# Optimization experiments

Hardware: AMD Instinct MI355X
Metric: run time of the kernel (lower is better)

Reference implementation:

```python
import jax, jax.numpy as jnp
import numpy as np

# e2m1 FP4 value table: sign bit in nibble MSB, values {0,0.5,1,1.5,2,3,4,6}
_E2M1 = jnp.array([0.0, 0.5, 1.0, 1.5, 2.0, 3.0, 4.0, 6.0,
                   -0.0, -0.5, -1.0, -1.5, -2.0, -3.0, -4.0, -6.0], dtype=jnp.float32)


def _dequant_fp4(packed, scales, group_size):
    """packed: [E, out, in//8] uint32; scales: [E, in//group_size, out] -> [E, out, in] f32."""
    shifts = jnp.arange(8, dtype=jnp.uint32) * 4  # nibble shift amounts 0,4,...,28
    nib = (packed[..., None] >> shifts) & jnp.uint32(0xF)  # [E, out, in//8, 8]
    E, O, P, _ = nib.shape
    nib = nib.reshape(E, O, P * 8).astype(jnp.int32)
    w = _E2M1[nib]  # [E, out, in] f32
    gids = jnp.arange(P * 8) // group_size  # group id per input column
    sc = jnp.transpose(scales, (0, 2, 1))[:, :, gids]  # [E, out, in]
    return w * sc


def setup_inputs() -> dict:
    E, H, I, T, K, G = 8, 2048, 1408, 2048, 2, 128
    key = jax.random.key(0)
    ks = jax.random.split(key, 9)
    x = jax.random.normal(ks[0], (T, H), dtype=jnp.float32)
    gate_packed = jax.random.bits(ks[1], (E, I, H // 8), dtype=jnp.uint32)
    up_packed = jax.random.bits(ks[2], (E, I, H // 8), dtype=jnp.uint32)
    down_packed = jax.random.bits(ks[3], (E, H, I // 8), dtype=jnp.uint32)
    gate_scales = jax.random.uniform(ks[4], (E, H // G, I), jnp.float32, 0.5, 1.5)
    up_scales = jax.random.uniform(ks[5], (E, H // G, I), jnp.float32, 0.5, 1.5)
    down_scales = jax.random.uniform(ks[6], (E, I // G, H), jnp.float32, 0.5, 1.5)
    topk_idx = jax.random.randint(ks[7], (T, K), 0, E, dtype=jnp.int32)
    w = jax.random.uniform(ks[8], (T, K), jnp.float32)
    topk_w = w / jnp.sum(w, axis=-1, keepdims=True)
    return {"x": x,
            "gate_packed": gate_packed, "gate_scales": gate_scales,
            "up_packed": up_packed, "up_scales": up_scales,
            "down_packed": down_packed, "down_scales": down_scales,
            "topk_idx": topk_idx, "topk_w": topk_w, "group_size": G}


def reference(x, gate_packed, gate_scales, up_packed, up_scales,
              down_packed, down_scales, topk_idx, topk_w, group_size):
    # Fused dequant (nibble unpack + e2m1 table + per-group scale) for all experts
    gate_w = _dequant_fp4(gate_packed, gate_scales, group_size)  # [E, I, H]
    up_w = _dequant_fp4(up_packed, up_scales, group_size)        # [E, I, H]
    down_w = _dequant_fp4(down_packed, down_scales, group_size)  # [E, H, I]
    # Grouped SwiGLU expert MLP (dense over E=8 experts, gather routed outputs)
    g = jnp.einsum('th,eih->eti', x, gate_w)
    u = jnp.einsum('th,eih->eti', x, up_w)
    h = jax.nn.silu(g) * u                                        # [E, T, I]
    y = jnp.einsum('eti,ehi->eth', h, down_w)                     # [E, T, H]
    T = x.shape[0]
    sel = y[topk_idx, jnp.arange(T)[:, None], :]                  # [T, K, H]
    return jnp.sum(sel * topk_w[..., None], axis=1)               # [T, H]
```

## Files before the change

kernel.cpp:

```cpp
#include <hip/hip_runtime.h>
#include <hip/hip_bf16.h>
#include <stdint.h>

#define E_ 8
#define H_ 2048
#define I_ 1408
#define T_ 2048
#define K_ 2
#define G_ 128

typedef __bf16 bf16;
typedef bf16 bf16x8 __attribute__((ext_vector_type(8)));
typedef float f32x4 __attribute__((ext_vector_type(4)));

__device__ __forceinline__ uint32_t prm(uint32_t hi, uint32_t lo, uint32_t sel) {
    return __builtin_amdgcn_perm(hi, lo, sel);
}

struct DequantTab { uint32_t thi0, thi1, tlo0, tlo1; };

__device__ __forceinline__ DequantTab build_tab(float s) {
    union { bf16 h[8]; uint32_t u[4]; } tb;
    tb.h[0] = (bf16)(0.0f);
    tb.h[1] = (bf16)(0.5f * s);
    tb.h[2] = (bf16)(1.0f * s);
    tb.h[3] = (bf16)(1.5f * s);
    tb.h[4] = (bf16)(2.0f * s);
    tb.h[5] = (bf16)(3.0f * s);
    tb.h[6] = (bf16)(4.0f * s);
    tb.h[7] = (bf16)(6.0f * s);
    DequantTab t;
    t.thi0 = prm(tb.u[1], tb.u[0], 0x07050301u);
    t.tlo0 = prm(tb.u[1], tb.u[0], 0x06040200u);
    t.thi1 = prm(tb.u[3], tb.u[2], 0x07050301u);
    t.tlo1 = prm(tb.u[3], tb.u[2], 0x06040200u);
    return t;
}

__device__ __forceinline__ uint4 dequant8t(uint32_t p, const DequantTab& t) {
    const uint32_t pr = p >> 4;
    const uint32_t pe = p  & 0x07070707u;
    const uint32_t po = pr & 0x07070707u;
    const uint32_t He = prm(t.thi1, t.thi0, pe) | ((p  & 0x08080808u) << 4);
    const uint32_t Le = prm(t.tlo1, t.tlo0, pe);
    const uint32_t Ho = prm(t.thi1, t.thi0, po) | ((pr & 0x08080808u) << 4);
    const uint32_t Lo = prm(t.tlo1, t.tlo0, po);
    const uint32_t E01 = prm(He, Le, 0x05010400u);
    const uint32_t E23 = prm(He, Le, 0x07030602u);
    const uint32_t O01 = prm(Ho, Lo, 0x05010400u);
    const uint32_t O23 = prm(Ho, Lo, 0x07030602u);
    return make_uint4(prm(O01, E01, 0x05040100u),
                      prm(O01, E01, 0x07060302u),
                      prm(O23, E23, 0x05040100u),
                      prm(O23, E23, 0x07060302u));
}

__device__ __forceinline__ void gld16(void* lds, const void* g) {
    __builtin_amdgcn_global_load_lds(
        (__attribute__((address_space(1))) void*)g,
        (__attribute__((address_space(3))) void*)lds, 16, 0, 0);
}

__global__ void route_count(const int* __restrict__ topk_idx, int* __restrict__ counts) {
    int p = blockIdx.x * blockDim.x + threadIdx.x;
    if (p < T_ * K_) atomicAdd(&counts[topk_idx[p]], 1);
}

__global__ void route_scan(const int* __restrict__ counts, int* __restrict__ offsets,
                           int* __restrict__ tmap) {
    if (threadIdx.x == 0) {
        int acc = 0, ti = 0;
        for (int e = 0; e < E_; e++) {
            offsets[e] = acc;
            int nt = (counts[e] + 127) >> 7;
            for (int j = 0; j < nt; j++) tmap[ti++] = (e << 16) | j;
            acc += counts[e];
        }
        offsets[E_] = acc;
        for (; ti < 64; ti++) tmap[ti] = -1;
    }
}

__global__ void route_fill(const int* __restrict__ topk_idx, const float* __restrict__ topk_w,
                           int* __restrict__ cursors, const int* __restrict__ offsets,
                           int* __restrict__ tok, float* __restrict__ wgt,
                           int* __restrict__ inv) {
    int p = blockIdx.x * blockDim.x + threadIdx.x;
    if (p < T_ * K_) {
        int e = topk_idx[p];
        int slot = atomicAdd(&cursors[e], 1);
        int idx = offsets[e] + slot;
        tok[idx] = p / K_;
        wgt[idx] = topk_w[p];
        inv[p] = idx;
    }
}

__global__ __launch_bounds__(256)
void xcast_kernel(const float* __restrict__ x, uint4* __restrict__ xb) {
    const int i = blockIdx.x * 256 + threadIdx.x;
    const float4 a = ((const float4*)x)[i * 2];
    const float4 b = ((const float4*)x)[i * 2 + 1];
    union { uint4 u; bf16 h[8]; } r;
    r.h[0] = (bf16)a.x; r.h[1] = (bf16)a.y; r.h[2] = (bf16)a.z; r.h[3] = (bf16)a.w;
    r.h[4] = (bf16)b.x; r.h[5] = (bf16)b.y; r.h[6] = (bf16)b.z; r.h[7] = (bf16)b.w;
    xb[i] = r.u;
}

__global__ __launch_bounds__(256, 3)
void gemm1t_kernel(const bf16* __restrict__ xb,
                   const uint32_t* __restrict__ gate_packed,
                   const float* __restrict__ gate_scales,
                   const uint32_t* __restrict__ up_packed,
                   const float* __restrict__ up_scales,
                   const int* __restrict__ offsets,
                   const int* __restrict__ tmap,
                   const int* __restrict__ tok, bf16* __restrict__ h_buf)
{
    const int tm = tmap[blockIdx.x];
    if (tm < 0) return;
    const int e = tm >> 16, ty = tm & 0xffff;
    const int row0 = offsets[e];
    const int cnt = offsets[e + 1] - row0;
    const int itile = blockIdx.y;

    __shared__ __align__(16) bf16 xs[2][128][64];
    __shared__ __align__(16) bf16 wgs[64][64];
    __shared__ __align__(16) bf16 wus[64][64];

    const int tid = threadIdx.x;

    const int xr = tid >> 3;
    const int xc = tid & 7;
    const int xch = (xc ^ (xr & 7)) * 8;
    const bf16* xsrc[4];
    bf16* xdst[4];
#pragma unroll
    for (int j = 0; j < 4; ++j) {
        int g = ty * 128 + xr + j * 32;
        g = (g < cnt) ? g : (cnt - 1);
        xsrc[j] = xb + (size_t)tok[row0 + g] * H_ + xch;
        xdst[j] = &xs[0][xr + j * 32][xc * 8];
    }

    const int mat  = tid >> 7;
    const int id   = tid & 127;
    const int wrow = id >> 1;
    const int quad = id & 1;
    const int irow = itile * 64 + wrow;
    const uint32_t* wp_row = (mat ? up_packed : gate_packed)
        + (size_t)e * I_ * (H_ / 8) + (size_t)irow * (H_ / 8) + quad * 4;
    const float* ws_row = (mat ? up_scales : gate_scales)
        + (size_t)e * (H_ / G_) * I_ + irow;
    bf16 (* const wdst)[64] = mat ? wus : wgs;

    const int wave = tid >> 6, lane = tid & 63;
    const int wy = wave >> 1, wx = wave & 1;
    const int lrow = lane & 15, kq = lane >> 4;

    f32x4 accg[4][2] = {};
    f32x4 accu[4][2] = {};

    float sc_cur = ws_row[0];
    uint4 pw = *(const uint4*)(wp_row);
#pragma unroll
    for (int j = 0; j < 4; ++j) gld16(xdst[j], xsrc[j]);

    constexpr int NG = H_ / G_;
    constexpr int NT = 2 * NG;
    for (int kg = 0; kg < NG; ++kg) {
        const int kgn = (kg + 1 < NG) ? kg + 1 : kg;
        const float sc_nxt = ws_row[(size_t)kgn * I_];
        const DequantTab tw = build_tab(sc_cur);
#pragma unroll
        for (int kh2 = 0; kh2 < 2; ++kh2) {
            const int t  = kg * 2 + kh2;
            const int tn = (t < NT - 1) ? t + 1 : t;
            const uint4 pwn = *(const uint4*)(wp_row + tn * 8);
#pragma unroll
            for (int j = 0; j < 4; ++j)
                gld16(xdst[j] + (kh2 ^ 1) * (128 * 64), xsrc[j] + tn * 64);
            __builtin_amdgcn_sched_barrier(0);
            {
                uint4 d0 = dequant8t(pw.x, tw);
                uint4 d1 = dequant8t(pw.y, tw);
                uint4 d2 = dequant8t(pw.z, tw);
                uint4 d3 = dequant8t(pw.w, tw);
                const int cb = quad * 4, rs = wrow & 7;
                *(uint4*)&wdst[wrow][((cb + 0) ^ rs) * 8] = d0;
                *(uint4*)&wdst[wrow][((cb + 1) ^ rs) * 8] = d1;
                *(uint4*)&wdst[wrow][((cb + 2) ^ rs) * 8] = d2;
                *(uint4*)&wdst[wrow][((cb + 3) ^ rs) * 8] = d3;
            }
            __builtin_amdgcn_sched_barrier(0);
            if (kh2 == 0) asm volatile("s_waitcnt vmcnt(6) lgkmcnt(0)" ::: "memory");
            else          asm volatile("s_waitcnt vmcnt(5) lgkmcnt(0)" ::: "memory");
            __builtin_amdgcn_s_barrier();
            __builtin_amdgcn_sched_barrier(0);
#pragma unroll
            for (int kh = 0; kh < 2; ++kh) {
                bf16x8 a[4], bg[2], bu[2];
#pragma unroll
                for (int mi = 0; mi < 4; ++mi) {
                    const int ra = wy * 64 + mi * 16 + lrow;
                    a[mi] = *(const bf16x8*)&xs[kh2][ra][((kh * 4 + kq) ^ (ra & 7)) * 8];
                }
#pragma unroll
                for (int ni = 0; ni < 2; ++ni) {
                    const int rb = wx * 32 + ni * 16 + lrow;
                    const int cb2 = ((kh * 4 + kq) ^ (rb & 7)) * 8;
                    bg[ni] = *(const bf16x8*)&wgs[rb][cb2];
                    bu[ni] = *(const bf16x8*)&wus[rb][cb2];
                }
#pragma unroll
                for (int mi = 0; mi < 4; ++mi)
#pragma unroll
                    for (int ni = 0; ni < 2; ++ni) {
                        accg[mi][ni] = __builtin_amdgcn_mfma_f32_16x16x32_bf16(a[mi], bg[ni], accg[mi][ni], 0, 0, 0);
                        accu[mi][ni] = __builtin_amdgcn_mfma_f32_16x16x32_bf16(a[mi], bu[ni], accu[mi][ni], 0, 0, 0);
                    }
            }
            __builtin_amdgcn_sched_barrier(0);
            asm volatile("s_waitcnt lgkmcnt(0)" ::: "memory");
            __builtin_amdgcn_s_barrier();
            pw = pwn;
        }
        sc_cur = sc_nxt;
    }

#pragma unroll
    for (int mi = 0; mi < 4; ++mi)
#pragma unroll
        for (int ni = 0; ni < 2; ++ni) {
            const int icol = itile * 64 + wx * 32 + ni * 16 + lrow;
#pragma unroll
            for (int r = 0; r < 4; ++r) {
                const int grow = ty * 128 + wy * 64 + mi * 16 + kq * 4 + r;
                if (grow < cnt) {
                    const float gv = accg[mi][ni][r];
                    const float hv = gv / (1.f + __expf(-gv)) * accu[mi][ni][r];
                    h_buf[(size_t)(row0 + grow) * I_ + icol] = (bf16)hv;
                }
            }
        }
}

__global__ __launch_bounds__(256, 3)
void gemm2t_kernel(const bf16* __restrict__ h_buf,
                   const uint32_t* __restrict__ down_packed,
                   const float* __restrict__ down_scales,
                   const int* __restrict__ offsets,
                   const int* __restrict__ tmap,
                   const float* __restrict__ wgt, float* __restrict__ yp)
{
    const int tm = tmap[blockIdx.x];
    if (tm < 0) return;
    const int e = tm >> 16, ty = tm & 0xffff;
    const int row0 = offsets[e];
    const int cnt = offsets[e + 1] - row0;
    const int htile = blockIdx.y;

    __shared__ __align__(16) bf16 hs[2][128][64];
    __shared__ __align__(16) bf16 wds[128][64];

    const int tid = threadIdx.x;

    const int xr = tid >> 3;
    const int xc = tid & 7;
    const int xch = (xc ^ (xr & 7)) * 8;
    const bf16* hsrc[4];
    bf16* hdst[4];
#pragma unroll
    for (int j = 0; j < 4; ++j) {
        int g = ty * 128 + xr + j * 32;
        g = (g < cnt) ? g : (cnt - 1);
        hsrc[j] = h_buf + (size_t)(row0 + g) * I_ + xch;
        hdst[j] = &hs[0][xr + j * 32][xc * 8];
    }

    const int wrow = tid >> 1;
    const int quad = tid & 1;
    const int hrow = htile * 128 + wrow;
    const uint32_t* dp_row = down_packed + (size_t)e * H_ * (I_ / 8) + (size_t)hrow * (I_ / 8) + quad * 4;
    const float* ds_row = down_scales + (size_t)e * (I_ / G_) * H_ + hrow;

    const int wave = tid >> 6, lane = tid & 63;
    const int wy = wave >> 1, wx = wave & 1;
    const int lrow = lane & 15, kq = lane >> 4;

    f32x4 acc[4][4] = {};

    float sc_cur = ds_row[0];
    uint4 pw = *(const uint4*)(dp_row);
#pragma unroll
    for (int j = 0; j < 4; ++j) gld16(hdst[j], hsrc[j]);

    constexpr int NG = I_ / G_;
    constexpr int NT = 2 * NG;
    for (int kg = 0; kg < NG; ++kg) {
        const int kgn = (kg + 1 < NG) ? kg + 1 : kg;
        const float sc_nxt = ds_row[(size_t)kgn * H_];
        const DequantTab td = build_tab(sc_cur);
#pragma unroll
        for (int kh2 = 0; kh2 < 2; ++kh2) {
            const int t  = kg * 2 + kh2;
            const int tn = (t < NT - 1) ? t + 1 : t;
            const uint4 pwn = *(const uint4*)(dp_row + tn * 8);
#pragma unroll
            for (int j = 0; j < 4; ++j)
                gld16(hdst[j] + (kh2 ^ 1) * (128 * 64), hsrc[j] + tn * 64);
            __builtin_amdgcn_sched_barrier(0);
            {
                uint4 d0 = dequant8t(pw.x, td);
                uint4 d1 = dequant8t(pw.y, td);
                uint4 d2 = dequant8t(pw.z, td);
                uint4 d3 = dequant8t(pw.w, td);
                const int cb = quad * 4, rs = wrow & 7;
                *(uint4*)&wds[wrow][((cb + 0) ^ rs) * 8] = d0;
                *(uint4*)&wds[wrow][((cb + 1) ^ rs) * 8] = d1;
                *(uint4*)&wds[wrow][((cb + 2) ^ rs) * 8] = d2;
                *(uint4*)&wds[wrow][((cb + 3) ^ rs) * 8] = d3;
            }
            __builtin_amdgcn_sched_barrier(0);
            if (kh2 == 0) asm volatile("s_waitcnt vmcnt(6) lgkmcnt(0)" ::: "memory");
            else          asm volatile("s_waitcnt vmcnt(5) lgkmcnt(0)" ::: "memory");
            __builtin_amdgcn_s_barrier();
            __builtin_amdgcn_sched_barrier(0);
#pragma unroll
            for (int kh = 0; kh < 2; ++kh) {
                bf16x8 a[4], b[4];
#pragma unroll
                for (int mi = 0; mi < 4; ++mi) {
                    const int ra = wy * 64 + mi * 16 + lrow;
                    a[mi] = *(const bf16x8*)&hs[kh2][ra][((kh * 4 + kq) ^ (ra & 7)) * 8];
                }
#pragma unroll
                for (int ni = 0; ni < 4; ++ni) {
                    const int rb = wx * 64 + ni * 16 + lrow;
                    b[ni] = *(const bf16x8*)&wds[rb][((kh * 4 + kq) ^ (rb & 7)) * 8];
                }
#pragma unroll
                for (int mi = 0; mi < 4; ++mi)
#pragma unroll
                    for (int ni = 0; ni < 4; ++ni)
                        acc[mi][ni] = __builtin_amdgcn_mfma_f32_16x16x32_bf16(a[mi], b[ni], acc[mi][ni], 0, 0, 0);
            }
            __builtin_amdgcn_sched_barrier(0);
            asm volatile("s_waitcnt lgkmcnt(0)" ::: "memory");
            __builtin_amdgcn_s_barrier();
            pw = pwn;
        }
        sc_cur = sc_nxt;
    }

#pragma unroll
    for (int mi = 0; mi < 4; ++mi)
#pragma unroll
        for (int r = 0; r < 4; ++r) {
            const int grow = ty * 128 + wy * 64 + mi * 16 + kq * 4 + r;
            if (grow < cnt) {
                const float w = wgt[row0 + grow];
#pragma unroll
                for (int ni = 0; ni < 4; ++ni) {
                    const int col = htile * 128 + wx * 64 + ni * 16 + lrow;
                    yp[(size_t)(row0 + grow) * H_ + col] = acc[mi][ni][r] * w;
                }
            }
        }
}

__global__ __launch_bounds__(256)
void combine_kernel(const float* __restrict__ yp, const int* __restrict__ inv,
                    float* __restrict__ out) {
    const int idx = blockIdx.x * 256 + threadIdx.x;
    const int t = idx >> 9;
    const int c = idx & 511;
    const float4 a = ((const float4*)yp)[(size_t)inv[t * 2] * (H_ / 4) + c];
    const float4 b = ((const float4*)yp)[(size_t)inv[t * 2 + 1] * (H_ / 4) + c];
    float4 o;
    o.x = a.x + b.x; o.y = a.y + b.y; o.z = a.z + b.z; o.w = a.w + b.w;
    ((float4*)out)[idx] = o;
}

extern "C" void kernel_launch(void* const* d_in, const int* in_sizes, int n_in,
                              void* d_out, int out_size, void* d_ws, size_t ws_size,
                              hipStream_t stream) {
    const float* x = (const float*)d_in[0];
    const uint32_t* gate_packed = (const uint32_t*)d_in[1];
    const float* gate_scales = (const float*)d_in[2];
    const uint32_t* up_packed = (const uint32_t*)d_in[3];
    const float* up_scales = (const float*)d_in[4];
    const uint32_t* down_packed = (const uint32_t*)d_in[5];
    const float* down_scales = (const float*)d_in[6];
    const int* topk_idx = (const int*)d_in[7];
    const float* topk_w = (const float*)d_in[8];
    float* out = (float*)d_out;

    char* ws = (char*)d_ws;
    int* counts  = (int*)ws;
    int* cursors = (int*)(ws + 32);
    int* offsets = (int*)(ws + 64);
    int* tmap    = (int*)(ws + 128);
    int* tok     = (int*)(ws + 640);
    float* wgt   = (float*)(ws + 17024);
    int* inv     = (int*)(ws + 33408);
    bf16* h_buf  = (bf16*)(ws + 49792);
    bf16* xb     = (bf16*)(ws + 49792 + 11534336ull);
    float* yp    = (float*)(ws + 49792 + 11534336ull + 8388608ull);

    hipMemsetAsync(d_ws, 0, 1024, stream);

    route_count<<<(T_ * K_ + 255) / 256, 256, 0, stream>>>(topk_idx, counts);
    route_scan<<<1, 64, 0, stream>>>(counts, offsets, tmap);
    route_fill<<<(T_ * K_ + 255) / 256, 256, 0, stream>>>(topk_idx, topk_w, cursors, offsets,
                                                          tok, wgt, inv);
    xcast_kernel<<<T_ * H_ / 8 / 256, 256, 0, stream>>>(x, (uint4*)xb);

    dim3 g1(40, I_ / 64);
    gemm1t_kernel<<<g1, 256, 0, stream>>>(xb, gate_packed, gate_scales, up_packed, up_scales,
                                          offsets, tmap, tok, h_buf);
    dim3 g2(40, H_ / 128);
    gemm2t_kernel<<<g2, 256, 0, stream>>>(h_buf, down_packed, down_scales,
                                          offsets, tmap, wgt, yp);
    combine_kernel<<<T_ * H_ / 4 / 256, 256, 0, stream>>>(yp, inv, out);
}
```

Measured before the change: 271.6 us.

## Dequantize FP4 weights directly into MFMA B-fragments and remap grid per expert

Each lane now loads the packed FP4 words for its own MFMA B operand and dequantizes them straight into registers. This removes the shared-memory staging of dequantized weights and one barrier/LDS round trip per k-step, but each row's dequant is repeated across the waves that share it. The tile map becomes a fixed 5 slots per expert, with the last slot looping over any extra 128-token chunks. The 1D grid puts the expert index in the low bits of the block id, presumably to interleave experts across XCDs/CUs. If one expert gets many tokens, the blocks in its last slot serialize that work.

```diff
diff --git a/kernel.cpp b/kernel.cpp
--- a/kernel.cpp
+++ b/kernel.cpp
@@ -55,12 +55,20 @@
                       prm(O23, E23, 0x07060302u));
 }
 
+__device__ __forceinline__ bf16x8 dq_frag(uint32_t p, const DequantTab& t) {
+    union { uint4 u; bf16x8 v; } r;
+    r.u = dequant8t(p, t);
+    return r.v;
+}
+
 __device__ __forceinline__ void gld16(void* lds, const void* g) {
     __builtin_amdgcn_global_load_lds(
         (__attribute__((address_space(1))) void*)g,
         (__attribute__((address_space(3))) void*)lds, 16, 0, 0);
 }
 
+#define SB0() __builtin_amdgcn_sched_barrier(0)
+
 __global__ void route_count(const int* __restrict__ topk_idx, int* __restrict__ counts) {
     int p = blockIdx.x * blockDim.x + threadIdx.x;
     if (p < T_ * K_) atomicAdd(&counts[topk_idx[p]], 1);
@@ -69,15 +77,15 @@
 __global__ void route_scan(const int* __restrict__ counts, int* __restrict__ offsets,
                            int* __restrict__ tmap) {
     if (threadIdx.x == 0) {
-        int acc = 0, ti = 0;
+        int acc = 0;
+        for (int e = 0; e < E_; e++) { offsets[e] = acc; acc += counts[e]; }
+        offsets[E_] = acc;
+        for (int s = 0; s < 40; s++) tmap[s] = -1;
         for (int e = 0; e < E_; e++) {
-            offsets[e] = acc;
             int nt = (counts[e] + 127) >> 7;
-            for (int j = 0; j < nt; j++) tmap[ti++] = (e << 16) | j;
-            acc += counts[e];
-        }
-        offsets[E_] = acc;
-        for (; ti < 64; ti++) tmap[ti] = -1;
+            if (nt > 5) nt = 5;
+            for (int j = 0; j < nt; j++) tmap[e * 5 + j] = (e << 16) | j;
+        }
     }
 }
 
@@ -117,132 +125,170 @@
                    const int* __restrict__ tmap,
                    const int* __restrict__ tok, bf16* __restrict__ h_buf)
 {
-    const int tm = tmap[blockIdx.x];
+    const int bid = blockIdx.x;
+    const int x8 = bid & 7;
+    const int r = bid >> 3;
+    const int t5 = r / 22;
+    const int itile = r - t5 * 22;
+    const int tm = tmap[x8 * 5 + t5];
     if (tm < 0) return;
-    const int e = tm >> 16, ty = tm & 0xffff;
+    const int e = tm >> 16, j0 = tm & 0xffff;
     const int row0 = offsets[e];
     const int cnt = offsets[e + 1] - row0;
-    const int itile = blockIdx.y;
+    const int nch = (cnt + 127) >> 7;
+    const int chend = (j0 == 4) ? nch : (j0 + 1);
 
     __shared__ __align__(16) bf16 xs[2][128][64];
-    __shared__ __align__(16) bf16 wgs[64][64];
-    __shared__ __align__(16) bf16 wus[64][64];
 
     const int tid = threadIdx.x;
+    const int wave = tid >> 6, lane = tid & 63;
+    const int wy = wave >> 1, wx = wave & 1;
+    const int lrow = lane & 15, kq = lane >> 4;
+
+    const uint32_t* gp = gate_packed + (size_t)e * I_ * (H_ / 8);
+    const uint32_t* upp = up_packed + (size_t)e * I_ * (H_ / 8);
+    const float* gsc = gate_scales + (size_t)e * (H_ / G_) * I_;
+    const float* usc = up_scales + (size_t)e * (H_ / G_) * I_;
+    int rb[2], wo[2];
+    rb[0] = itile * 64 + wx * 32 + lrow;
+    rb[1] = rb[0] + 16;
+    wo[0] = rb[0] * (H_ / 8) + kq;
+    wo[1] = rb[1] * (H_ / 8) + kq;
 
     const int xr = tid >> 3;
     const int xc = tid & 7;
     const int xch = (xc ^ (xr & 7)) * 8;
-    const bf16* xsrc[4];
-    bf16* xdst[4];
-#pragma unroll
-    for (int j = 0; j < 4; ++j) {
-        int g = ty * 128 + xr + j * 32;
-        g = (g < cnt) ? g : (cnt - 1);
-        xsrc[j] = xb + (size_t)tok[row0 + g] * H_ + xch;
-        xdst[j] = &xs[0][xr + j * 32][xc * 8];
-    }
-
-    const int mat  = tid >> 7;
-    const int id   = tid & 127;
-    const int wrow = id >> 1;
-    const int quad = id & 1;
-    const int irow = itile * 64 + wrow;
-    const uint32_t* wp_row = (mat ? up_packed : gate_packed)
-        + (size_t)e * I_ * (H_ / 8) + (size_t)irow * (H_ / 8) + quad * 4;
-    const float* ws_row = (mat ? up_scales : gate_scales)
-        + (size_t)e * (H_ / G_) * I_ + irow;
-    bf16 (* const wdst)[64] = mat ? wus : wgs;
-
-    const int wave = tid >> 6, lane = tid & 63;
-    const int wy = wave >> 1, wx = wave & 1;
-    const int lrow = lane & 15, kq = lane >> 4;
-
-    f32x4 accg[4][2] = {};
-    f32x4 accu[4][2] = {};
-
-    float sc_cur = ws_row[0];
-    uint4 pw = *(const uint4*)(wp_row);
-#pragma unroll
-    for (int j = 0; j < 4; ++j) gld16(xdst[j], xsrc[j]);
 
     constexpr int NG = H_ / G_;
     constexpr int NT = 2 * NG;
-    for (int kg = 0; kg < NG; ++kg) {
-        const int kgn = (kg + 1 < NG) ? kg + 1 : kg;
-        const float sc_nxt = ws_row[(size_t)kgn * I_];
-        const DequantTab tw = build_tab(sc_cur);
-#pragma unroll
-        for (int kh2 = 0; kh2 < 2; ++kh2) {
-            const int t  = kg * 2 + kh2;
-            const int tn = (t < NT - 1) ? t + 1 : t;
-            const uint4 pwn = *(const uint4*)(wp_row + tn * 8);
-#pragma unroll
-            for (int j = 0; j < 4; ++j)
-                gld16(xdst[j] + (kh2 ^ 1) * (128 * 64), xsrc[j] + tn * 64);
-            __builtin_amdgcn_sched_barrier(0);
-            {
-                uint4 d0 = dequant8t(pw.x, tw);
-                uint4 d1 = dequant8t(pw.y, tw);
-                uint4 d2 = dequant8t(pw.z, tw);
-                uint4 d3 = dequant8t(pw.w, tw);
-                const int cb = quad * 4, rs = wrow & 7;
-                *(uint4*)&wdst[wrow][((cb + 0) ^ rs) * 8] = d0;
-                *(uint4*)&wdst[wrow][((cb + 1) ^ rs) * 8] = d1;
-                *(uint4*)&wdst[wrow][((cb + 2) ^ rs) * 8] = d2;
-                *(uint4*)&wdst[wrow][((cb + 3) ^ rs) * 8] = d3;
+
+    for (int ch = j0; ch < chend; ++ch) {
+        const bf16* xsrc[4];
+        bf16* xdst[4];
+#pragma unroll
+        for (int j = 0; j < 4; ++j) {
+            int g = ch * 128 + xr + j * 32;
+            g = (g < cnt) ? g : (cnt - 1);
+            xsrc[j] = xb + (size_t)tok[row0 + g] * H_ + xch;
+            xdst[j] = &xs[0][xr + j * 32][xc * 8];
+        }
+
+        f32x4 accg[4][2] = {};
+        f32x4 accu[4][2] = {};
+        uint32_t pwc[2][2][2], pwn[2][2][2];
+        float scc[2][2], scn[2][2];
+
+#pragma unroll
+        for (int j = 0; j < 4; ++j) gld16(xdst[j], xsrc[j]);
+        SB0();
+#pragma unroll
+        for (int ni = 0; ni < 2; ++ni)
+#pragma unroll
+            for (int kh = 0; kh < 2; ++kh) {
+                pwc[0][ni][kh] = gp[wo[ni] + kh * 4];
+                pwc[1][ni][kh] = upp[wo[ni] + kh * 4];
             }
-            __builtin_amdgcn_sched_barrier(0);
-            if (kh2 == 0) asm volatile("s_waitcnt vmcnt(6) lgkmcnt(0)" ::: "memory");
-            else          asm volatile("s_waitcnt vmcnt(5) lgkmcnt(0)" ::: "memory");
-            __builtin_amdgcn_s_barrier();
-            __builtin_amdgcn_sched_barrier(0);
-#pragma unroll
-            for (int kh = 0; kh < 2; ++kh) {
-                bf16x8 a[4], bg[2], bu[2];
-#pragma unroll
-                for (int mi = 0; mi < 4; ++mi) {
-                    const int ra = wy * 64 + mi * 16 + lrow;
-                    a[mi] = *(const bf16x8*)&xs[kh2][ra][((kh * 4 + kq) ^ (ra & 7)) * 8];
-                }
-#pragma unroll
-                for (int ni = 0; ni < 2; ++ni) {
-                    const int rb = wx * 32 + ni * 16 + lrow;
-                    const int cb2 = ((kh * 4 + kq) ^ (rb & 7)) * 8;
-                    bg[ni] = *(const bf16x8*)&wgs[rb][cb2];
-                    bu[ni] = *(const bf16x8*)&wus[rb][cb2];
-                }
-#pragma unroll
-                for (int mi = 0; mi < 4; ++mi)
+#pragma unroll
+        for (int ni = 0; ni < 2; ++ni) {
+            scc[0][ni] = gsc[rb[ni]];
+            scc[1][ni] = usc[rb[ni]];
+        }
+        SB0();
+        asm volatile("s_waitcnt vmcnt(12) lgkmcnt(0)" ::: "memory");
+        __builtin_amdgcn_s_barrier();
+        SB0();
+
+        for (int kg = 0; kg < NG; ++kg) {
+            DequantTab tab[2][2];
+#pragma unroll
+            for (int mat = 0; mat < 2; ++mat)
+#pragma unroll
+                for (int ni = 0; ni < 2; ++ni)
+                    tab[mat][ni] = build_tab(scc[mat][ni]);
+#pragma unroll
+            for (int kh2 = 0; kh2 < 2; ++kh2) {
+                const int t = kg * 2 + kh2;
+                if (t < NT - 1) {
+                    const int tn = t + 1;
+#pragma unroll
+                    for (int j = 0; j < 4; ++j)
+                        gld16(xdst[j] + (kh2 ^ 1) * (128 * 64), xsrc[j] + tn * 64);
+                    SB0();
+#pragma unroll
+                    for (int ni = 0; ni < 2; ++ni)
+#pragma unroll
+                        for (int kh = 0; kh < 2; ++kh) {
+                            pwn[0][ni][kh] = gp[wo[ni] + tn * 8 + kh * 4];
+                            pwn[1][ni][kh] = upp[wo[ni] + tn * 8 + kh * 4];
+                        }
+                    if (kh2 == 0) {
+                        const int kgn = (kg + 1 < NG) ? kg + 1 : kg;
+#pragma unroll
+                        for (int ni = 0; ni < 2; ++ni) {
+                            scn[0][ni] = gsc[kgn * I_ + rb[ni]];
+                            scn[1][ni] = usc[kgn * I_ + rb[ni]];
+                        }
+                    }
+                    SB0();
+                }
+#pragma unroll
+                for (int kh = 0; kh < 2; ++kh) {
+                    bf16x8 a[4], bg[2], bu[2];
+#pragma unroll
+                    for (int mi = 0; mi < 4; ++mi) {
+                        const int ra = wy * 64 + mi * 16 + lrow;
+                        a[mi] = *(const bf16x8*)&xs[kh2][ra][((kh * 4 + kq) ^ (ra & 7)) * 8];
+                    }
 #pragma unroll
                     for (int ni = 0; ni < 2; ++ni) {
-                        accg[mi][ni] = __builtin_amdgcn_mfma_f32_16x16x32_bf16(a[mi], bg[ni], accg[mi][ni], 0, 0, 0);
-                        accu[mi][ni] = __builtin_amdgcn_mfma_f32_16x16x32_bf16(a[mi], bu[ni], accu[mi][ni], 0, 0, 0);
-                    }
+                        bg[ni] = dq_frag(pwc[0][ni][kh], tab[0][ni]);
+                        bu[ni] = dq_frag(pwc[1][ni][kh], tab[1][ni]);
+                    }
+#pragma unroll
+                    for (int mi = 0; mi < 4; ++mi)
+#pragma unroll
+                        for (int ni = 0; ni < 2; ++ni) {
+                            accg[mi][ni] = __builtin_amdgcn_mfma_f32_16x16x32_bf16(a[mi], bg[ni], accg[mi][ni], 0, 0, 0);
+                            accu[mi][ni] = __builtin_amdgcn_mfma_f32_16x16x32_bf16(a[mi], bu[ni], accu[mi][ni], 0, 0, 0);
+                        }
+                }
+                SB0();
+                if (t == NT - 1)      asm volatile("s_waitcnt vmcnt(0) lgkmcnt(0)" ::: "memory");
+                else if (kh2 == 0)    asm volatile("s_waitcnt vmcnt(12) lgkmcnt(0)" ::: "memory");
+                else                  asm volatile("s_waitcnt vmcnt(8) lgkmcnt(0)" ::: "memory");
+                __builtin_amdgcn_s_barrier();
+                SB0();
+#pragma unroll
+                for (int mat = 0; mat < 2; ++mat)
+#pragma unroll
+                    for (int ni = 0; ni < 2; ++ni)
+#pragma unroll
+                        for (int kh = 0; kh < 2; ++kh)
+                            pwc[mat][ni][kh] = pwn[mat][ni][kh];
             }
-            __builtin_amdgcn_sched_barrier(0);
-            asm volatile("s_waitcnt lgkmcnt(0)" ::: "memory");
-            __builtin_amdgcn_s_barrier();
-            pw = pwn;
-        }
-        sc_cur = sc_nxt;
+#pragma unroll
+            for (int mat = 0; mat < 2; ++mat)
+#pragma unroll
+                for (int ni = 0; ni < 2; ++ni)
+                    scc[mat][ni] = scn[mat][ni];
+        }
+
+#pragma unroll
+        for (int mi = 0; mi < 4; ++mi)
+#pragma unroll
+            for (int ni = 0; ni < 2; ++ni) {
+                const int icol = itile * 64 + wx * 32 + ni * 16 + lrow;
+#pragma unroll
+                for (int rr = 0; rr < 4; ++rr) {
+                    const int grow = ch * 128 + wy * 64 + mi * 16 + kq * 4 + rr;
+                    if (grow < cnt) {
+                        const float gv = accg[mi][ni][rr];
+                        const float hv = gv / (1.f + __expf(-gv)) * accu[mi][ni][rr];
+                        h_buf[(size_t)(row0 + grow) * I_ + icol] = (bf16)hv;
+                    }
+                }
+            }
     }
-
-#pragma unroll
-    for (int mi = 0; mi < 4; ++mi)
-#pragma unroll
-        for (int ni = 0; ni < 2; ++ni) {
-            const int icol = itile * 64 + wx * 32 + ni * 16 + lrow;
-#pragma unroll
-            for (int r = 0; r < 4; ++r) {
-                const int grow = ty * 128 + wy * 64 + mi * 16 + kq * 4 + r;
-                if (grow < cnt) {
-                    const float gv = accg[mi][ni][r];
-                    const float hv = gv / (1.f + __expf(-gv)) * accu[mi][ni][r];
-                    h_buf[(size_t)(row0 + grow) * I_ + icol] = (bf16)hv;
-                }
-            }
-        }
 }
 
 __global__ __launch_bounds__(256, 3)
@@ -253,120 +299,145 @@
                    const int* __restrict__ tmap,
                    const float* __restrict__ wgt, float* __restrict__ yp)
 {
-    const int tm = tmap[blockIdx.x];
+    const int bid = blockIdx.x;
+    const int x8 = bid & 7;
+    const int r = bid >> 3;
+    const int t5 = r >> 4;
+    const int htile = r & 15;
+    const int tm = tmap[x8 * 5 + t5];
     if (tm < 0) return;
-    const int e = tm >> 16, ty = tm & 0xffff;
+    const int e = tm >> 16, j0 = tm & 0xffff;
     const int row0 = offsets[e];
     const int cnt = offsets[e + 1] - row0;
-    const int htile = blockIdx.y;
+    const int nch = (cnt + 127) >> 7;
+    const int chend = (j0 == 4) ? nch : (j0 + 1);
 
     __shared__ __align__(16) bf16 hs[2][128][64];
-    __shared__ __align__(16) bf16 wds[128][64];
 
     const int tid = threadIdx.x;
+    const int wave = tid >> 6, lane = tid & 63;
+    const int wy = wave >> 1, wx = wave & 1;
+    const int lrow = lane & 15, kq = lane >> 4;
+
+    const uint32_t* dp = down_packed + (size_t)e * H_ * (I_ / 8);
+    const float* dsc = down_scales + (size_t)e * (I_ / G_) * H_;
+    int rb[4], wo[4];
+#pragma unroll
+    for (int ni = 0; ni < 4; ++ni) {
+        rb[ni] = htile * 128 + wx * 64 + ni * 16 + lrow;
+        wo[ni] = rb[ni] * (I_ / 8) + kq;
+    }
 
     const int xr = tid >> 3;
     const int xc = tid & 7;
     const int xch = (xc ^ (xr & 7)) * 8;
-    const bf16* hsrc[4];
-    bf16* hdst[4];
-#pragma unroll
-    for (int j = 0; j < 4; ++j) {
-        int g = ty * 128 + xr + j * 32;
-        g = (g < cnt) ? g : (cnt - 1);
-        hsrc[j] = h_buf + (size_t)(row0 + g) * I_ + xch;
-        hdst[j] = &hs[0][xr + j * 32][xc * 8];
-    }
-
-    const int wrow = tid >> 1;
-    const int quad = tid & 1;
-    const int hrow = htile * 128 + wrow;
-    const uint32_t* dp_row = down_packed + (size_t)e * H_ * (I_ / 8) + (size_t)hrow * (I_ / 8) + quad * 4;
-    const float* ds_row = down_scales + (size_t)e * (I_ / G_) * H_ + hrow;
-
-    const int wave = tid >> 6, lane = tid & 63;
-    const int wy = wave >> 1, wx = wave & 1;
-    const int lrow = lane & 15, kq = lane >> 4;
-
-    f32x4 acc[4][4] = {};
-
-    float sc_cur = ds_row[0];
-    uint4 pw = *(const uint4*)(dp_row);
-#pragma unroll
-    for (int j = 0; j < 4; ++j) gld16(hdst[j], hsrc[j]);
 
     constexpr int NG = I_ / G_;
     constexpr int NT = 2 * NG;
-    for (int kg = 0; kg < NG; ++kg) {
-        const int kgn = (kg + 1 < NG) ? kg + 1 : kg;
-        const float sc_nxt = ds_row[(size_t)kgn * H_];
-        const DequantTab td = build_tab(sc_cur);
-#pragma unroll
-        for (int kh2 = 0; kh2 < 2; ++kh2) {
-            const int t  = kg * 2 + kh2;
-            const int tn = (t < NT - 1) ? t + 1 : t;
-            const uint4 pwn = *(const uint4*)(dp_row + tn * 8);
-#pragma unroll
-            for (int j = 0; j < 4; ++j)
-                gld16(hdst[j] + (kh2 ^ 1) * (128 * 64), hsrc[j] + tn * 64);
-            __builtin_amdgcn_sched_barrier(0);
-            {
-                uint4 d0 = dequant8t(pw.x, td);
-                uint4 d1 = dequant8t(pw.y, td);
-                uint4 d2 = dequant8t(pw.z, td);
-                uint4 d3 = dequant8t(pw.w, td);
-                const int cb = quad * 4, rs = wrow & 7;
-                *(uint4*)&wds[wrow][((cb + 0) ^ rs) * 8] = d0;
-                *(uint4*)&wds[wrow][((cb + 1) ^ rs) * 8] = d1;
-                *(uint4*)&wds[wrow][((cb + 2) ^ rs) * 8] = d2;
-                *(uint4*)&wds[wrow][((cb + 3) ^ rs) * 8] = d3;
+
+    for (int ch = j0; ch < chend; ++ch) {
+        const bf16* hsrc[4];
+        bf16* hdst[4];
+#pragma unroll
+        for (int j = 0; j < 4; ++j) {
+            int g = ch * 128 + xr + j * 32;
+            g = (g < cnt) ? g : (cnt - 1);
+            hsrc[j] = h_buf + (size_t)(row0 + g) * I_ + xch;
+            hdst[j] = &hs[0][xr + j * 32][xc * 8];
+        }
+
+        f32x4 acc[4][4] = {};
+        uint32_t pwc[4][2], pwn[4][2];
+        float scc[4], scn[4];
+
+#pragma unroll
+        for (int j = 0; j < 4; ++j) gld16(hdst[j], hsrc[j]);
+        SB0();
+#pragma unroll
+        for (int ni = 0; ni < 4; ++ni)
+#pragma unroll
+            for (int kh = 0; kh < 2; ++kh)
+                pwc[ni][kh] = dp[wo[ni] + kh * 4];
+#pragma unroll
+        for (int ni = 0; ni < 4; ++ni) scc[ni] = dsc[rb[ni]];
+        SB0();
+        asm volatile("s_waitcnt vmcnt(12) lgkmcnt(0)" ::: "memory");
+        __builtin_amdgcn_s_barrier();
+        SB0();
+
+        for (int kg = 0; kg < NG; ++kg) {
+            DequantTab tab[4];
+#pragma unroll
+            for (int ni = 0; ni < 4; ++ni) tab[ni] = build_tab(scc[ni]);
+#pragma unroll
+            for (int kh2 = 0; kh2 < 2; ++kh2) {
+                const int t = kg * 2 + kh2;
+                if (t < NT - 1) {
+                    const int tn = t + 1;
+#pragma unroll
+                    for (int j = 0; j < 4; ++j)
+                        gld16(hdst[j] + (kh2 ^ 1) * (128 * 64), hsrc[j] + tn * 64);
+                    SB0();
+#pragma unroll
+                    for (int ni = 0; ni < 4; ++ni)
+#pragma unroll
+                        for (int kh = 0; kh < 2; ++kh)
+                            pwn[ni][kh] = dp[wo[ni] + tn * 8 + kh * 4];
+                    if (kh2 == 0) {
+                        const int kgn = (kg + 1 < NG) ? kg + 1 : kg;
+#pragma unroll
+                        for (int ni = 0; ni < 4; ++ni) scn[ni] = dsc[kgn * H_ + rb[ni]];
+                    }
+                    SB0();
+                }
+#pragma unroll
+                for (int kh = 0; kh < 2; ++kh) {
+                    bf16x8 a[4], b[4];
+#pragma unroll
+                    for (int mi = 0; mi < 4; ++mi) {
+                        const int ra = wy * 64 + mi * 16 + lrow;
+                        a[mi] = *(const bf16x8*)&hs[kh2][ra][((kh * 4 + kq) ^ (ra & 7)) * 8];
+                    }
+#pragma unroll
+                    for (int ni = 0; ni < 4; ++ni)
+                        b[ni] = dq_frag(pwc[ni][kh], tab[ni]);
+#pragma unroll
+                    for (int mi = 0; mi < 4; ++mi)
+#pragma unroll
+                        for (int ni = 0; ni < 4; ++ni)
+                            acc[mi][ni] = __builtin_amdgcn_mfma_f32_16x16x32_bf16(a[mi], b[ni], acc[mi][ni], 0, 0, 0);
+                }
+                SB0();
+                if (t == NT - 1)      asm volatile("s_waitcnt vmcnt(0) lgkmcnt(0)" ::: "memory");
+                else if (kh2 == 0)    asm volatile("s_waitcnt vmcnt(12) lgkmcnt(0)" ::: "memory");
+                else                  asm volatile("s_waitcnt vmcnt(8) lgkmcnt(0)" ::: "memory");
+                __builtin_amdgcn_s_barrier();
+                SB0();
+#pragma unroll
+                for (int ni = 0; ni < 4; ++ni)
+#pragma unroll
+                    for (int kh = 0; kh < 2; ++kh)
+                        pwc[ni][kh] = pwn[ni][kh];
             }
-            __builtin_amdgcn_sched_barrier(0);
-            if (kh2 == 0) asm volatile("s_waitcnt vmcnt(6) lgkmcnt(0)" ::: "memory");
-            else          asm volatile("s_waitcnt vmcnt(5) lgkmcnt(0)" ::: "memory");
-            __builtin_amdgcn_s_barrier();
-            __builtin_amdgcn_sched_barrier(0);
-#pragma unroll
-            for (int kh = 0; kh < 2; ++kh) {
-                bf16x8 a[4], b[4];
-#pragma unroll
-                for (int mi = 0; mi < 4; ++mi) {
-                    const int ra = wy * 64 + mi * 16 + lrow;
-                    a[mi] = *(const bf16x8*)&hs[kh2][ra][((kh * 4 + kq) ^ (ra & 7)) * 8];
-                }
-#pragma unroll
-                for (int ni = 0; ni < 4; ++ni) {
-                    const int rb = wx * 64 + ni * 16 + lrow;
-                    b[ni] = *(const bf16x8*)&wds[rb][((kh * 4 + kq) ^ (rb & 7)) * 8];
-                }
-#pragma unroll
-                for (int mi = 0; mi < 4; ++mi)
-#pragma unroll
-                    for (int ni = 0; ni < 4; ++ni)
-                        acc[mi][ni] = __builtin_amdgcn_mfma_f32_16x16x32_bf16(a[mi], b[ni], acc[mi][ni], 0, 0, 0);
+#pragma unroll
+            for (int ni = 0; ni < 4; ++ni) scc[ni] = scn[ni];
+        }
+
+#pragma unroll
+        for (int mi = 0; mi < 4; ++mi)
+#pragma unroll
+            for (int rr = 0; rr < 4; ++rr) {
+                const int grow = ch * 128 + wy * 64 + mi * 16 + kq * 4 + rr;
+                if (grow < cnt) {
+                    const float w = wgt[row0 + grow];
+#pragma unroll
+                    for (int ni = 0; ni < 4; ++ni) {
+                        const int col = htile * 128 + wx * 64 + ni * 16 + lrow;
+                        yp[(size_t)(row0 + grow) * H_ + col] = acc[mi][ni][rr] * w;
+                    }
+                }
             }
-            __builtin_amdgcn_sched_barrier(0);
-            asm volatile("s_waitcnt lgkmcnt(0)" ::: "memory");
-            __builtin_amdgcn_s_barrier();
-            pw = pwn;
-        }
-        sc_cur = sc_nxt;
     }
-
-#pragma unroll
-    for (int mi = 0; mi < 4; ++mi)
-#pragma unroll
-        for (int r = 0; r < 4; ++r) {
-            const int grow = ty * 128 + wy * 64 + mi * 16 + kq * 4 + r;
-            if (grow < cnt) {
-                const float w = wgt[row0 + grow];
-#pragma unroll
-                for (int ni = 0; ni < 4; ++ni) {
-                    const int col = htile * 128 + wx * 64 + ni * 16 + lrow;
-                    yp[(size_t)(row0 + grow) * H_ + col] = acc[mi][ni][r] * w;
-                }
-            }
-        }
 }
 
 __global__ __launch_bounds__(256)
@@ -416,11 +487,10 @@
                                                           tok, wgt, inv);
     xcast_kernel<<<T_ * H_ / 8 / 256, 256, 0, stream>>>(x, (uint4*)xb);
 
-    dim3 g1(40, I_ / 64);
-    gemm1t_kernel<<<g1, 256, 0, stream>>>(xb, gate_packed, gate_scales, up_packed, up_scales,
-                                          offsets, tmap, tok, h_buf);
-    dim3 g2(40, H_ / 128);
-    gemm2t_kernel<<<g2, 256, 0, stream>>>(h_buf, down_packed, down_scales,
-                                          offsets, tmap, wgt, yp);
+    gemm1t_kernel<<<dim3(110 * 8), 256, 0, stream>>>(xb, gate_packed, gate_scales,
+                                                     up_packed, up_scales,
+                                                     offsets, tmap, tok, h_buf);
+    gemm2t_kernel<<<dim3(80 * 8), 256, 0, stream>>>(h_buf, down_packed, down_scales,
+                                                    offsets, tmap, wgt, yp);
     combine_kernel<<<T_ * H_ / 4 / 256, 256, 0, stream>>>(yp, inv, out);
 }
```

New measurement: 410.3 us. 1.51x slower.

## Double-buffer dequantized weight tiles to overlap dequant with MFMA and halve barriers

Applied to the files above, without the earlier changes.

Both grouped GEMM kernels now keep two LDS buffers for the dequantized weight tiles as well as the activation tiles. The dequant of the next k-slice is written into the alternate buffer while MFMAs consume the current one, so each slice needs one barrier instead of two. Launch bounds drop from 3 to 2 blocks per CU to fit the extra LDS and registers, which trades occupancy for the better overlap.

```diff
diff --git a/kernel.cpp b/kernel.cpp
--- a/kernel.cpp
+++ b/kernel.cpp
@@ -61,6 +61,19 @@
         (__attribute__((address_space(3))) void*)lds, 16, 0, 0);
 }
 
+#define SB0() __builtin_amdgcn_sched_barrier(0)
+
+#define DQW(WD, PW, TAB) do { \
+    uint4 d0_ = dequant8t((PW).x, (TAB)); \
+    uint4 d1_ = dequant8t((PW).y, (TAB)); \
+    uint4 d2_ = dequant8t((PW).z, (TAB)); \
+    uint4 d3_ = dequant8t((PW).w, (TAB)); \
+    *(uint4*)&WD[wrow][((cb + 0) ^ rs) * 8] = d0_; \
+    *(uint4*)&WD[wrow][((cb + 1) ^ rs) * 8] = d1_; \
+    *(uint4*)&WD[wrow][((cb + 2) ^ rs) * 8] = d2_; \
+    *(uint4*)&WD[wrow][((cb + 3) ^ rs) * 8] = d3_; \
+} while (0)
+
 __global__ void route_count(const int* __restrict__ topk_idx, int* __restrict__ counts) {
     int p = blockIdx.x * blockDim.x + threadIdx.x;
     if (p < T_ * K_) atomicAdd(&counts[topk_idx[p]], 1);
@@ -107,7 +120,7 @@
     xb[i] = r.u;
 }
 
-__global__ __launch_bounds__(256, 3)
+__global__ __launch_bounds__(256, 2)
 void gemm1t_kernel(const bf16* __restrict__ xb,
                    const uint32_t* __restrict__ gate_packed,
                    const float* __restrict__ gate_scales,
@@ -124,9 +137,12 @@
     const int cnt = offsets[e + 1] - row0;
     const int itile = blockIdx.y;
 
-    __shared__ __align__(16) bf16 xs[2][128][64];
-    __shared__ __align__(16) bf16 wgs[64][64];
-    __shared__ __align__(16) bf16 wus[64][64];
+    __shared__ __align__(16) bf16 xs0[128][64];
+    __shared__ __align__(16) bf16 xs1[128][64];
+    __shared__ __align__(16) bf16 wgs0[64][64];
+    __shared__ __align__(16) bf16 wgs1[64][64];
+    __shared__ __align__(16) bf16 wus0[64][64];
+    __shared__ __align__(16) bf16 wus1[64][64];
 
     const int tid = threadIdx.x;
 
@@ -134,25 +150,28 @@
     const int xc = tid & 7;
     const int xch = (xc ^ (xr & 7)) * 8;
     const bf16* xsrc[4];
-    bf16* xdst[4];
+    bf16 *xdst0[4], *xdst1[4];
 #pragma unroll
     for (int j = 0; j < 4; ++j) {
         int g = ty * 128 + xr + j * 32;
         g = (g < cnt) ? g : (cnt - 1);
         xsrc[j] = xb + (size_t)tok[row0 + g] * H_ + xch;
-        xdst[j] = &xs[0][xr + j * 32][xc * 8];
+        xdst0[j] = &xs0[xr + j * 32][xc * 8];
+        xdst1[j] = &xs1[xr + j * 32][xc * 8];
     }
 
     const int mat  = tid >> 7;
     const int id   = tid & 127;
     const int wrow = id >> 1;
     const int quad = id & 1;
+    const int cb = quad * 4, rs = wrow & 7;
     const int irow = itile * 64 + wrow;
     const uint32_t* wp_row = (mat ? up_packed : gate_packed)
         + (size_t)e * I_ * (H_ / 8) + (size_t)irow * (H_ / 8) + quad * 4;
     const float* ws_row = (mat ? up_scales : gate_scales)
         + (size_t)e * (H_ / G_) * I_ + irow;
-    bf16 (* const wdst)[64] = mat ? wus : wgs;
+    bf16 (* const wd0)[64] = mat ? wus0 : wgs0;
+    bf16 (* const wd1)[64] = mat ? wus1 : wgs1;
 
     const int wave = tid >> 6, lane = tid & 63;
     const int wy = wave >> 1, wx = wave & 1;
@@ -161,71 +180,87 @@
     f32x4 accg[4][2] = {};
     f32x4 accu[4][2] = {};
 
-    float sc_cur = ws_row[0];
-    uint4 pw = *(const uint4*)(wp_row);
-#pragma unroll
-    for (int j = 0; j < 4; ++j) gld16(xdst[j], xsrc[j]);
-
     constexpr int NG = H_ / G_;
-    constexpr int NT = 2 * NG;
+
+#define MFMA1(XS, WG, WU) do { \
+    _Pragma("unroll") \
+    for (int kh = 0; kh < 2; ++kh) { \
+        bf16x8 a[4], bg[2], bu[2]; \
+        _Pragma("unroll") \
+        for (int mi = 0; mi < 4; ++mi) { \
+            const int ra = wy * 64 + mi * 16 + lrow; \
+            a[mi] = *(const bf16x8*)&XS[ra][((kh * 4 + kq) ^ (ra & 7)) * 8]; \
+        } \
+        _Pragma("unroll") \
+        for (int ni = 0; ni < 2; ++ni) { \
+            const int rbq = wx * 32 + ni * 16 + lrow; \
+            const int cbq = ((kh * 4 + kq) ^ (rbq & 7)) * 8; \
+            bg[ni] = *(const bf16x8*)&WG[rbq][cbq]; \
+            bu[ni] = *(const bf16x8*)&WU[rbq][cbq]; \
+        } \
+        _Pragma("unroll") \
+        for (int mi = 0; mi < 4; ++mi) \
+            _Pragma("unroll") \
+            for (int ni = 0; ni < 2; ++ni) { \
+                accg[mi][ni] = __builtin_amdgcn_mfma_f32_16x16x32_bf16(a[mi], bg[ni], accg[mi][ni], 0, 0, 0); \
+                accu[mi][ni] = __builtin_amdgcn_mfma_f32_16x16x32_bf16(a[mi], bu[ni], accu[mi][ni], 0, 0, 0); \
+            } \
+    } \
+} while (0)
+
+#pragma unroll
+    for (int j = 0; j < 4; ++j) gld16(xdst0[j], xsrc[j]);
+    SB0();
+    uint4 pw0 = *(const uint4*)(wp_row);
+    uint4 pwO = *(const uint4*)(wp_row + 8);
+    float sc0 = ws_row[0];
+    SB0();
+    DequantTab tab = build_tab(sc0);
+    DQW(wd0, pw0, tab);
+    asm volatile("s_waitcnt lgkmcnt(0)" ::: "memory");
+    __builtin_amdgcn_s_barrier();
+    SB0();
+
+    float scn = 0.f;
+    uint4 pwE;
     for (int kg = 0; kg < NG; ++kg) {
-        const int kgn = (kg + 1 < NG) ? kg + 1 : kg;
-        const float sc_nxt = ws_row[(size_t)kgn * I_];
-        const DequantTab tw = build_tab(sc_cur);
-#pragma unroll
-        for (int kh2 = 0; kh2 < 2; ++kh2) {
-            const int t  = kg * 2 + kh2;
-            const int tn = (t < NT - 1) ? t + 1 : t;
-            const uint4 pwn = *(const uint4*)(wp_row + tn * 8);
-#pragma unroll
-            for (int j = 0; j < 4; ++j)
-                gld16(xdst[j] + (kh2 ^ 1) * (128 * 64), xsrc[j] + tn * 64);
-            __builtin_amdgcn_sched_barrier(0);
-            {
-                uint4 d0 = dequant8t(pw.x, tw);
-                uint4 d1 = dequant8t(pw.y, tw);
-                uint4 d2 = dequant8t(pw.z, tw);
-                uint4 d3 = dequant8t(pw.w, tw);
-                const int cb = quad * 4, rs = wrow & 7;
-                *(uint4*)&wdst[wrow][((cb + 0) ^ rs) * 8] = d0;
-                *(uint4*)&wdst[wrow][((cb + 1) ^ rs) * 8] = d1;
-                *(uint4*)&wdst[wrow][((cb + 2) ^ rs) * 8] = d2;
-                *(uint4*)&wdst[wrow][((cb + 3) ^ rs) * 8] = d3;
-            }
-            __builtin_amdgcn_sched_barrier(0);
-            if (kh2 == 0) asm volatile("s_waitcnt vmcnt(6) lgkmcnt(0)" ::: "memory");
-            else          asm volatile("s_waitcnt vmcnt(5) lgkmcnt(0)" ::: "memory");
+        const bool last = (kg == NG - 1);
+#pragma unroll
+        for (int j = 0; j < 4; ++j) gld16(xdst1[j], xsrc[j] + (kg * 2 + 1) * 64);
+        SB0();
+        if (!last) {
+            pwE = *(const uint4*)(wp_row + (size_t)(kg * 2 + 2) * 8);
+            scn = ws_row[(size_t)(kg + 1) * I_];
+        }
+        SB0();
+        DQW(wd1, pwO, tab);
+        MFMA1(xs0, wgs0, wus0);
+        SB0();
+        if (!last) asm volatile("s_waitcnt vmcnt(2) lgkmcnt(0)" ::: "memory");
+        else       asm volatile("s_waitcnt vmcnt(0) lgkmcnt(0)" ::: "memory");
+        __builtin_amdgcn_s_barrier();
+        SB0();
+
+        if (!last) {
+#pragma unroll
+            for (int j = 0; j < 4; ++j) gld16(xdst0[j], xsrc[j] + (kg * 2 + 2) * 64);
+            SB0();
+            pwO = *(const uint4*)(wp_row + (size_t)(kg * 2 + 3) * 8);
+            SB0();
+            tab = build_tab(scn);
+            DQW(wd0, pwE, tab);
+            MFMA1(xs1, wgs1, wus1);
+            SB0();
+            asm volatile("s_waitcnt vmcnt(1) lgkmcnt(0)" ::: "memory");
             __builtin_amdgcn_s_barrier();
-            __builtin_amdgcn_sched_barrier(0);
-#pragma unroll
-            for (int kh = 0; kh < 2; ++kh) {
-                bf16x8 a[4], bg[2], bu[2];
-#pragma unroll
-                for (int mi = 0; mi < 4; ++mi) {
-                    const int ra = wy * 64 + mi * 16 + lrow;
-                    a[mi] = *(const bf16x8*)&xs[kh2][ra][((kh * 4 + kq) ^ (ra & 7)) * 8];
-                }
-#pragma unroll
-                for (int ni = 0; ni < 2; ++ni) {
-                    const int rb = wx * 32 + ni * 16 + lrow;
-                    const int cb2 = ((kh * 4 + kq) ^ (rb & 7)) * 8;
-                    bg[ni] = *(const bf16x8*)&wgs[rb][cb2];
-                    bu[ni] = *(const bf16x8*)&wus[rb][cb2];
-                }
-#pragma unroll
-                for (int mi = 0; mi < 4; ++mi)
-#pragma unroll
-                    for (int ni = 0; ni < 2; ++ni) {
-                        accg[mi][ni] = __builtin_amdgcn_mfma_f32_16x16x32_bf16(a[mi], bg[ni], accg[mi][ni], 0, 0, 0);
-                        accu[mi][ni] = __builtin_amdgcn_mfma_f32_16x16x32_bf16(a[mi], bu[ni], accu[mi][ni], 0, 0, 0);
-                    }
-            }
-            __builtin_amdgcn_sched_barrier(0);
+            SB0();
+        } else {
+            MFMA1(xs1, wgs1, wus1);
+            SB0();
             asm volatile("s_waitcnt lgkmcnt(0)" ::: "memory");
             __builtin_amdgcn_s_barrier();
-            pw = pwn;
-        }
-        sc_cur = sc_nxt;
+            SB0();
+        }
     }
 
 #pragma unroll
@@ -243,9 +278,10 @@
                 }
             }
         }
-}
-
-__global__ __launch_bounds__(256, 3)
+#undef MFMA1
+}
+
+__global__ __launch_bounds__(256, 2)
 void gemm2t_kernel(const bf16* __restrict__ h_buf,
                    const uint32_t* __restrict__ down_packed,
                    const float* __restrict__ down_scales,
@@ -260,8 +296,10 @@
     const int cnt = offsets[e + 1] - row0;
     const int htile = blockIdx.y;
 
-    __shared__ __align__(16) bf16 hs[2][128][64];
-    __shared__ __align__(16) bf16 wds[128][64];
+    __shared__ __align__(16) bf16 hs0[128][64];
+    __shared__ __align__(16) bf16 hs1[128][64];
+    __shared__ __align__(16) bf16 wds0[128][64];
+    __shared__ __align__(16) bf16 wds1[128][64];
 
     const int tid = threadIdx.x;
 
@@ -269,17 +307,19 @@
     const int xc = tid & 7;
     const int xch = (xc ^ (xr & 7)) * 8;
     const bf16* hsrc[4];
-    bf16* hdst[4];
+    bf16 *hdst0[4], *hdst1[4];
 #pragma unroll
     for (int j = 0; j < 4; ++j) {
         int g = ty * 128 + xr + j * 32;
         g = (g < cnt) ? g : (cnt - 1);
         hsrc[j] = h_buf + (size_t)(row0 + g) * I_ + xch;
-        hdst[j] = &hs[0][xr + j * 32][xc * 8];
+        hdst0[j] = &hs0[xr + j * 32][xc * 8];
+        hdst1[j] = &hs1[xr + j * 32][xc * 8];
     }
 
     const int wrow = tid >> 1;
     const int quad = tid & 1;
+    const int cb = quad * 4, rs = wrow & 7;
     const int hrow = htile * 128 + wrow;
     const uint32_t* dp_row = down_packed + (size_t)e * H_ * (I_ / 8) + (size_t)hrow * (I_ / 8) + quad * 4;
     const float* ds_row = down_scales + (size_t)e * (I_ / G_) * H_ + hrow;
@@ -290,74 +330,91 @@
 
     f32x4 acc[4][4] = {};
 
-    float sc_cur = ds_row[0];
-    uint4 pw = *(const uint4*)(dp_row);
-#pragma unroll
-    for (int j = 0; j < 4; ++j) gld16(hdst[j], hsrc[j]);
-
     constexpr int NG = I_ / G_;
-    constexpr int NT = 2 * NG;
+
+#define MFMA2(HS, WD) do { \
+    _Pragma("unroll") \
+    for (int kh = 0; kh < 2; ++kh) { \
+        bf16x8 a[4], b[4]; \
+        _Pragma("unroll") \
+        for (int mi = 0; mi < 4; ++mi) { \
+            const int ra = wy * 64 + mi * 16 + lrow; \
+            a[mi] = *(const bf16x8*)&HS[ra][((kh * 4 + kq) ^ (ra & 7)) * 8]; \
+        } \
+        _Pragma("unroll") \
+        for (int ni = 0; ni < 4; ++ni) { \
+            const int rbq = wx * 64 + ni * 16 + lrow; \
+            b[ni] = *(const bf16x8*)&WD[rbq][((kh * 4 + kq) ^ (rbq & 7)) * 8]; \
+        } \
+        _Pragma("unroll") \
+        for (int mi = 0; mi < 4; ++mi) \
+            _Pragma("unroll") \
+            for (int ni = 0; ni < 4; ++ni) \
+                acc[mi][ni] = __builtin_amdgcn_mfma_f32_16x16x32_bf16(a[mi], b[ni], acc[mi][ni], 0, 0, 0); \
+    } \
+} while (0)
+
+#pragma unroll
+    for (int j = 0; j < 4; ++j) gld16(hdst0[j], hsrc[j]);
+    SB0();
+    uint4 pw0 = *(const uint4*)(dp_row);
+    uint4 pwO = *(const uint4*)(dp_row + 8);
+    float sc0 = ds_row[0];
+    SB0();
+    DequantTab tab = build_tab(sc0);
+    DQW(wds0, pw0, tab);
+    asm volatile("s_waitcnt lgkmcnt(0)" ::: "memory");
+    __builtin_amdgcn_s_barrier();
+    SB0();
+
+    float scn = 0.f;
+    uint4 pwE;
     for (int kg = 0; kg < NG; ++kg) {
-        const int kgn = (kg + 1 < NG) ? kg + 1 : kg;
-        const float sc_nxt = ds_row[(size_t)kgn * H_];
-        const DequantTab td = build_tab(sc_cur);
-#pragma unroll
-        for (int kh2 = 0; kh2 < 2; ++kh2) {
-            const int t  = kg * 2 + kh2;
-            const int tn = (t < NT - 1) ? t + 1 : t;
-            const uint4 pwn = *(const uint4*)(dp_row + tn * 8);
-#pragma unroll
-            for (int j = 0; j < 4; ++j)
-                gld16(hdst[j] + (kh2 ^ 1) * (128 * 64), hsrc[j] + tn * 64);
-            __builtin_amdgcn_sched_barrier(0);
-            {
-                uint4 d0 = dequant8t(pw.x, td);
-                uint4 d1 = dequant8t(pw.y, td);
-                uint4 d2 = dequant8t(pw.z, td);
-                uint4 d3 = dequant8t(pw.w, td);
-                const int cb = quad * 4, rs = wrow & 7;
-                *(uint4*)&wds[wrow][((cb + 0) ^ rs) * 8] = d0;
-                *(uint4*)&wds[wrow][((cb + 1) ^ rs) * 8] = d1;
-                *(uint4*)&wds[wrow][((cb + 2) ^ rs) * 8] = d2;
-                *(uint4*)&wds[wrow][((cb + 3) ^ rs) * 8] = d3;
-            }
-            __builtin_amdgcn_sched_barrier(0);
-            if (kh2 == 0) asm volatile("s_waitcnt vmcnt(6) lgkmcnt(0)" ::: "memory");
-            else          asm volatile("s_waitcnt vmcnt(5) lgkmcnt(0)" ::: "memory");
+        const bool last = (kg == NG - 1);
+#pragma unroll
+        for (int j = 0; j < 4; ++j) gld16(hdst1[j], hsrc[j] + (kg * 2 + 1) * 64);
+        SB0();
+        if (!last) {
+            pwE = *(const uint4*)(dp_row + (size_t)(kg * 2 + 2) * 8);
+            scn = ds_row[(size_t)(kg + 1) * H_];
+        }
+        SB0();
+        DQW(wds1, pwO, tab);
+        MFMA2(hs0, wds0);
+        SB0();
+        if (!last) asm volatile("s_waitcnt vmcnt(2) lgkmcnt(0)" ::: "memory");
+        else       asm volatile("s_waitcnt vmcnt(0) lgkmcnt(0)" ::: "memory");
+        __builtin_amdgcn_s_barrier();
+        SB0();
+
+        if (!last) {
+#pragma unroll
+            for (int j = 0; j < 4; ++j) gld16(hdst0[j], hsrc[j] + (kg * 2 + 2) * 64);
+            SB0();
+            pwO = *(const uint4*)(dp_row + (size_t)(kg * 2 + 3) * 8);
+            SB0();
+            tab = build_tab(scn);
+            DQW(wds0, pwE, tab);
+            MFMA2(hs1, wds1);
+            SB0();
+            asm volatile("s_waitcnt vmcnt(1) lgkmcnt(0)" ::: "memory");
             __builtin_amdgcn_s_barrier();
-            __builtin_amdgcn_sched_barrier(0);
-#pragma unroll
-            for (int kh = 0; kh < 2; ++kh) {
-                bf16x8 a[4], b[4];
-#pragma unroll
-                for (int mi = 0; mi < 4; ++mi) {
-                    const int ra = wy * 64 + mi * 16 + lrow;
-                    a[mi] = *(const bf16x8*)&hs[kh2][ra][((kh * 4 + kq) ^ (ra & 7)) * 8];
-                }
-#pragma unroll
-                for (int ni = 0; ni < 4; ++ni) {
-                    const int rb = wx * 64 + ni * 16 + lrow;
-                    b[ni] = *(const bf16x8*)&wds[rb][((kh * 4 + kq) ^ (rb & 7)) * 8];
-                }
-#pragma unroll
-                for (int mi = 0; mi < 4; ++mi)
-#pragma unroll
-                    for (int ni = 0; ni < 4; ++ni)
-                        acc[mi][ni] = __builtin_amdgcn_mfma_f32_16x16x32_bf16(a[mi], b[ni], acc[mi][ni], 0, 0, 0);
-            }
-            __builtin_amdgcn_sched_barrier(0);
+            SB0();
+        } else {
+            MFMA2(hs1, wds1);
+            SB0();
             asm volatile("s_waitcnt lgkmcnt(0)" ::: "memory");
             __builtin_amdgcn_s_barrier();
-            pw = pwn;
-        }
-        sc_cur = sc_nxt;
+            SB0();
+        }
     }
 
 #pragma unroll
     for (int mi = 0; mi < 4; ++mi)
 #pragma unroll
         for (int r = 0; r < 4; ++r) {
-            const int grow = ty * 128 + wy * 64 + mi * 16 + kq * 4 + r;
+            const int lr = wy * 64 + mi * 16 + kq * 4 + r;
+            const int grow = ty * 128 + lr;
             if (grow < cnt) {
                 const float w = wgt[row0 + grow];
 #pragma unroll
@@ -367,6 +424,7 @@
                 }
             }
         }
+#undef MFMA2
 }
 
 __global__ __launch_bounds__(256)
```

Result: no change. 273.4 us (+0.7%).
